# Optimization experiments

Measured on AMD Instinct MI355X. Metric: run time of the kernel, lower is better.

## Reference

```python
import jax, jax.numpy as jnp
import numpy as np

MAX_DISP = 4  # max_displacement = pad_size = 4, stride_1 = stride_2 = 1, kernel_size = 1
NEG_SLOPE = 0.1


def setup_inputs() -> dict:
    key = jax.random.key(0)
    k1, k2 = jax.random.split(key)
    B, C, H, W = 8, 128, 128, 256
    x1 = jax.random.normal(k1, (B, C, H, W), dtype=jnp.float32)
    x2 = jax.random.normal(k2, (B, C, H, W), dtype=jnp.float32)
    return {"x1": x1, "x2": x2}


def reference(x1, x2):
    # FlowNet/PWC-Net correlation: for each displacement (dy, dx) in
    # [-MAX_DISP, MAX_DISP]^2, dot-product over channels (normalized by C),
    # giving (2*MAX_DISP+1)^2 = 81 output channels; then LeakyReLU(0.1).
    B, C, H, W = x1.shape
    pad = MAX_DISP
    x2p = jnp.pad(x2, ((0, 0), (0, 0), (pad, pad), (pad, pad)))  # [B,C,H+8,W+8]
    vols = []
    for dy in range(2 * MAX_DISP + 1):          # fixed small displacement set
        for dx in range(2 * MAX_DISP + 1):
            shifted = jax.lax.dynamic_slice(x2p, (0, 0, dy, dx), (B, C, H, W))
            vols.append(jnp.mean(x1 * shifted, axis=1))  # mean over channels
    cv = jnp.stack(vols, axis=1)                 # [B, 81, H, W]
    return jax.nn.leaky_relu(cv, NEG_SLOPE)
```

## Files before the change

### kernel.cpp

```cpp
#include <hip/hip_runtime.h>


constexpr int MAXD = 4;
constexpr int ND   = 9;
constexpr int NDISP = 81;
constexpr int Bb = 8, Cc = 128, Hh = 128, Ww = 256;
constexpr int TH = 8, TW = 64, NPIX = 8;
constexpr int CK = 4;
constexpr int NCHUNK = Cc / CK;
constexpr int XROWS = TH + 2 * MAXD;
constexpr int XSTR  = 76;
constexpr int CH_TILE = XROWS * XSTR;
constexpr int BUFF = CK * CH_TILE;
constexpr int NTHREADS = ND * 64;
constexpr int HW = Hh * Ww;
constexpr float SCALE = 1.0f / 128.0f;
constexpr float SLOPE = 0.1f;

__global__ __launch_bounds__(NTHREADS, 1)
void corr81_kernel(const float* __restrict__ x1, const float* __restrict__ x2,
                   float* __restrict__ out) {
  const int tid = threadIdx.x;
  const int wv  = tid >> 6;
  const int l   = tid & 63;
  const int r   = l >> 3;
  const int cb  = (l & 7) << 3;

  const int w0 = blockIdx.x * TW;
  const int h0 = blockIdx.y * TH;
  const int b  = blockIdx.z;

  __shared__ float x2s[2 * BUFF];

  const int srow = tid / 36;
  const int scol = (tid - srow * 36) * 2;
  const int gh2  = h0 - MAXD + srow;
  const int gw2  = w0 - MAXD + scol;
  const bool sok = (gh2 >= 0) && (gh2 < Hh) && (gw2 >= 0) && (gw2 < Ww);
  const int x2base = b * (Cc * HW) + gh2 * Ww + gw2;
  const int sldso  = srow * XSTR + scol;

  const int x1base = (b * Cc * Hh + h0 + r) * Ww + w0 + cb;
  const int ldro   = (r + wv) * XSTR + cb;

  float acc[ND][NPIX];
#pragma unroll
  for (int dx = 0; dx < ND; ++dx)
#pragma unroll
    for (int i = 0; i < NPIX; ++i) acc[dx][i] = 0.0f;

  float a[2][NPIX];

  auto loadx1 = [&](int ch, float* dst) {
    const float* p = x1 + x1base + ch * HW;
    float4 t0 = *reinterpret_cast<const float4*>(p);
    float4 t1 = *reinterpret_cast<const float4*>(p + 4);
    dst[0] = t0.x; dst[1] = t0.y; dst[2] = t0.z; dst[3] = t0.w;
    dst[4] = t1.x; dst[5] = t1.y; dst[6] = t1.z; dst[7] = t1.w;
  };

#pragma unroll
  for (int c = 0; c < CK; ++c) {
    float2 v = make_float2(0.0f, 0.0f);
    if (sok) v = *reinterpret_cast<const float2*>(x2 + x2base + c * HW);
    *reinterpret_cast<float2*>(&x2s[c * CH_TILE + sldso]) = v;
  }
  loadx1(0, a[0]);
  __syncthreads();

  for (int k = 0; k < NCHUNK; ++k) {
    const int kn = k + 1;
    float2 sreg[CK];
    if (kn < NCHUNK) {
#pragma unroll
      for (int c = 0; c < CK; ++c) {
        float2 v = make_float2(0.0f, 0.0f);
        if (sok) v = *reinterpret_cast<const float2*>(x2 + x2base + (kn * CK + c) * HW);
        sreg[c] = v;
      }
    }
    const float* lb = &x2s[(k & 1) * BUFF + ldro];
#pragma unroll
    for (int c = 0; c < CK; ++c) {
      const int ch = k * CK + c;
      int chn = ch + 1; if (chn >= Cc) chn = Cc - 1;
      loadx1(chn, a[(c + 1) & 1]);

      const float* lp = lb + c * CH_TILE;
      float4 q0 = *reinterpret_cast<const float4*>(lp);
      float4 q1 = *reinterpret_cast<const float4*>(lp + 4);
      float4 q2 = *reinterpret_cast<const float4*>(lp + 8);
      float4 q3 = *reinterpret_cast<const float4*>(lp + 12);
      float xr[16] = {q0.x, q0.y, q0.z, q0.w, q1.x, q1.y, q1.z, q1.w,
                      q2.x, q2.y, q2.z, q2.w, q3.x, q3.y, q3.z, q3.w};
      const float* av = a[c & 1];
#pragma unroll
      for (int dx = 0; dx < ND; ++dx)
#pragma unroll
        for (int i = 0; i < NPIX; ++i)
          acc[dx][i] = fmaf(av[i], xr[i + dx], acc[dx][i]);
    }
    if (kn < NCHUNK) {
#pragma unroll
      for (int c = 0; c < CK; ++c)
        *reinterpret_cast<float2*>(&x2s[(kn & 1) * BUFF + c * CH_TILE + sldso]) = sreg[c];
    }
    __syncthreads();
  }

  const int obase = (b * NDISP + wv * ND) * HW + (h0 + r) * Ww + w0 + cb;
#pragma unroll
  for (int dx = 0; dx < ND; ++dx) {
    float4 v0, v1;
    float t;
    t = acc[dx][0] * SCALE; v0.x = fmaxf(t, t * SLOPE);
    t = acc[dx][1] * SCALE; v0.y = fmaxf(t, t * SLOPE);
    t = acc[dx][2] * SCALE; v0.z = fmaxf(t, t * SLOPE);
    t = acc[dx][3] * SCALE; v0.w = fmaxf(t, t * SLOPE);
    t = acc[dx][4] * SCALE; v1.x = fmaxf(t, t * SLOPE);
    t = acc[dx][5] * SCALE; v1.y = fmaxf(t, t * SLOPE);
    t = acc[dx][6] * SCALE; v1.z = fmaxf(t, t * SLOPE);
    t = acc[dx][7] * SCALE; v1.w = fmaxf(t, t * SLOPE);
    float* po = out + obase + dx * HW;
    *reinterpret_cast<float4*>(po)     = v0;
    *reinterpret_cast<float4*>(po + 4) = v1;
  }
}

extern "C" void kernel_launch(void* const* d_in, const int* in_sizes, int n_in,
                              void* d_out, int out_size, void* d_ws, size_t ws_size,
                              hipStream_t stream) {
  const float* x1 = (const float*)d_in[0];
  const float* x2 = (const float*)d_in[1];
  float* out = (float*)d_out;
  dim3 grid(Ww / TW, Hh / TH, Bb);
  corr81_kernel<<<grid, NTHREADS, 0, stream>>>(x1, x2, out);
}
```

Baseline: 419.6 us.

## Remap lanes, widen x2 staging to float4, batch x1 loads per chunk

Lane mapping is transposed so each wavefront's 8 row-lanes are contiguous, which changes the LDS access pattern across banks. x2 staging switches from float2 to float4 loads, with two thread groups each covering two channels, so fewer global and LDS transactions are issued. x1 loads for all four channels of a chunk are issued up front, LDS reads are double-buffered in registers, and sched_barriers pin the ordering. This raises register pressure and changes the bounds check at the right tile edge.

```diff
diff --git a/kernel.cpp b/kernel.cpp
--- a/kernel.cpp
+++ b/kernel.cpp
@@ -23,22 +23,25 @@
   const int tid = threadIdx.x;
   const int wv  = tid >> 6;
   const int l   = tid & 63;
-  const int r   = l >> 3;
-  const int cb  = (l & 7) << 3;
+  const int r   = l & 7;
+  const int cb  = (l >> 3) << 3;
 
   const int w0 = blockIdx.x * TW;
   const int h0 = blockIdx.y * TH;
   const int b  = blockIdx.z;
 
-  __shared__ float x2s[2 * BUFF];
+  __shared__ __align__(16) float x2s[2 * BUFF];
 
-  const int srow = tid / 36;
-  const int scol = (tid - srow * 36) * 2;
+  const int cp   = tid / 288;
+  const int st   = tid - cp * 288;
+  const int srow = st / 18;
+  const int scol = (st - srow * 18) * 4;
   const int gh2  = h0 - MAXD + srow;
   const int gw2  = w0 - MAXD + scol;
-  const bool sok = (gh2 >= 0) && (gh2 < Hh) && (gw2 >= 0) && (gw2 < Ww);
+  const bool sok = (gh2 >= 0) && (gh2 < Hh) && (gw2 >= 0) && (gw2 + 3 < Ww + 1);
   const int x2base = b * (Cc * HW) + gh2 * Ww + gw2;
   const int sldso  = srow * XSTR + scol;
+  const int chp0   = cp * 2;
 
   const int x1base = (b * Cc * Hh + h0 + r) * Ww + w0 + cb;
   const int ldro   = (r + wv) * XSTR + cb;
@@ -49,61 +52,70 @@
 #pragma unroll
     for (int i = 0; i < NPIX; ++i) acc[dx][i] = 0.0f;
 
-  float a[2][NPIX];
-
-  auto loadx1 = [&](int ch, float* dst) {
-    const float* p = x1 + x1base + ch * HW;
-    float4 t0 = *reinterpret_cast<const float4*>(p);
-    float4 t1 = *reinterpret_cast<const float4*>(p + 4);
-    dst[0] = t0.x; dst[1] = t0.y; dst[2] = t0.z; dst[3] = t0.w;
-    dst[4] = t1.x; dst[5] = t1.y; dst[6] = t1.z; dst[7] = t1.w;
+  auto ldx2 = [](const float* lp, float* dst) {
+    float4 q0 = *reinterpret_cast<const float4*>(lp);
+    float4 q1 = *reinterpret_cast<const float4*>(lp + 4);
+    float4 q2 = *reinterpret_cast<const float4*>(lp + 8);
+    float4 q3 = *reinterpret_cast<const float4*>(lp + 12);
+    dst[0]  = q0.x; dst[1]  = q0.y; dst[2]  = q0.z; dst[3]  = q0.w;
+    dst[4]  = q1.x; dst[5]  = q1.y; dst[6]  = q1.z; dst[7]  = q1.w;
+    dst[8]  = q2.x; dst[9]  = q2.y; dst[10] = q2.z; dst[11] = q2.w;
+    dst[12] = q3.x; dst[13] = q3.y; dst[14] = q3.z; dst[15] = q3.w;
   };
 
 #pragma unroll
-  for (int c = 0; c < CK; ++c) {
-    float2 v = make_float2(0.0f, 0.0f);
-    if (sok) v = *reinterpret_cast<const float2*>(x2 + x2base + c * HW);
-    *reinterpret_cast<float2*>(&x2s[c * CH_TILE + sldso]) = v;
+  for (int j = 0; j < 2; ++j) {
+    float4 v = make_float4(0.0f, 0.0f, 0.0f, 0.0f);
+    if (sok) v = *reinterpret_cast<const float4*>(x2 + x2base + (chp0 + j) * HW);
+    *reinterpret_cast<float4*>(&x2s[(chp0 + j) * CH_TILE + sldso]) = v;
   }
-  loadx1(0, a[0]);
   __syncthreads();
 
+#pragma unroll 1
   for (int k = 0; k < NCHUNK; ++k) {
     const int kn = k + 1;
-    float2 sreg[CK];
+
+    float a4[CK][NPIX];
+#pragma unroll
+    for (int c = 0; c < CK; ++c) {
+      const float* p = x1 + x1base + (k * CK + c) * HW;
+      float4 t0 = *reinterpret_cast<const float4*>(p);
+      float4 t1 = *reinterpret_cast<const float4*>(p + 4);
+      a4[c][0] = t0.x; a4[c][1] = t0.y; a4[c][2] = t0.z; a4[c][3] = t0.w;
+      a4[c][4] = t1.x; a4[c][5] = t1.y; a4[c][6] = t1.z; a4[c][7] = t1.w;
+    }
+    __builtin_amdgcn_sched_barrier(0);
+
+    float4 sreg[2];
     if (kn < NCHUNK) {
 #pragma unroll
-      for (int c = 0; c < CK; ++c) {
-        float2 v = make_float2(0.0f, 0.0f);
-        if (sok) v = *reinterpret_cast<const float2*>(x2 + x2base + (kn * CK + c) * HW);
-        sreg[c] = v;
+      for (int j = 0; j < 2; ++j) {
+        float4 v = make_float4(0.0f, 0.0f, 0.0f, 0.0f);
+        if (sok) v = *reinterpret_cast<const float4*>(x2 + x2base + (kn * CK + chp0 + j) * HW);
+        sreg[j] = v;
       }
     }
+    __builtin_amdgcn_sched_barrier(0);
+
     const float* lb = &x2s[(k & 1) * BUFF + ldro];
+    float xr[2][16];
+    ldx2(lb, xr[0]);
 #pragma unroll
     for (int c = 0; c < CK; ++c) {
-      const int ch = k * CK + c;
-      int chn = ch + 1; if (chn >= Cc) chn = Cc - 1;
-      loadx1(chn, a[(c + 1) & 1]);
-
-      const float* lp = lb + c * CH_TILE;
-      float4 q0 = *reinterpret_cast<const float4*>(lp);
-      float4 q1 = *reinterpret_cast<const float4*>(lp + 4);
-      float4 q2 = *reinterpret_cast<const float4*>(lp + 8);
-      float4 q3 = *reinterpret_cast<const float4*>(lp + 12);
-      float xr[16] = {q0.x, q0.y, q0.z, q0.w, q1.x, q1.y, q1.z, q1.w,
-                      q2.x, q2.y, q2.z, q2.w, q3.x, q3.y, q3.z, q3.w};
-      const float* av = a[c & 1];
+      if (c + 1 < CK) ldx2(lb + (c + 1) * CH_TILE, xr[(c + 1) & 1]);
+      const float* av = a4[c];
+      const float* xv = xr[c & 1];
 #pragma unroll
       for (int dx = 0; dx < ND; ++dx)
 #pragma unroll
         for (int i = 0; i < NPIX; ++i)
-          acc[dx][i] = fmaf(av[i], xr[i + dx], acc[dx][i]);
+          acc[dx][i] = fmaf(av[i], xv[i + dx], acc[dx][i]);
     }
+
     if (kn < NCHUNK) {
 #pragma unroll
-      for (int c = 0; c < CK; ++c)
-        *reinterpret_cast<float2*>(&x2s[(kn & 1) * BUFF + c * CH_TILE + sldso]) = sreg[c];
+      for (int j = 0; j < 2; ++j)
+        *reinterpret_cast<float4*>(&x2s[(kn & 1) * BUFF + (chp0 + j) * CH_TILE + sldso]) = sreg[j];
     }
     __syncthreads();
   }
```

After: 597.9 us. 42.5% more time.

## Load x2 windows directly from global memory, dropping LDS staging and barriers

Applied to the files above, without the earlier changes.

Removes the shared-memory double-buffered x2 tile and the per-chunk __syncthreads, and has each thread read its 16-wide x2 window straight from global memory with float4 loads, relying on L1/L2 for reuse across the 9 waves. Channels are software-pipelined two at a time in registers. This drops LDS traffic and block-wide synchronization, but it puts redundant global/cache loads on every wave, and float4 loads at offset cb-4 may be unaligned or zero-masked at the edges.

```diff
diff --git a/kernel.cpp b/kernel.cpp
--- a/kernel.cpp
+++ b/kernel.cpp
@@ -6,12 +6,6 @@
 constexpr int NDISP = 81;
 constexpr int Bb = 8, Cc = 128, Hh = 128, Ww = 256;
 constexpr int TH = 8, TW = 64, NPIX = 8;
-constexpr int CK = 4;
-constexpr int NCHUNK = Cc / CK;
-constexpr int XROWS = TH + 2 * MAXD;
-constexpr int XSTR  = 76;
-constexpr int CH_TILE = XROWS * XSTR;
-constexpr int BUFF = CK * CH_TILE;
 constexpr int NTHREADS = ND * 64;
 constexpr int HW = Hh * Ww;
 constexpr float SCALE = 1.0f / 128.0f;
@@ -30,18 +24,19 @@
   const int h0 = blockIdx.y * TH;
   const int b  = blockIdx.z;
 
-  __shared__ float x2s[2 * BUFF];
+  const int x1base = (b * Cc * Hh + h0 + r) * Ww + w0 + cb;
 
-  const int srow = tid / 36;
-  const int scol = (tid - srow * 36) * 2;
-  const int gh2  = h0 - MAXD + srow;
-  const int gw2  = w0 - MAXD + scol;
-  const bool sok = (gh2 >= 0) && (gh2 < Hh) && (gw2 >= 0) && (gw2 < Ww);
-  const int x2base = b * (Cc * HW) + gh2 * Ww + gw2;
-  const int sldso  = srow * XSTR + scol;
-
-  const int x1base = (b * Cc * Hh + h0 + r) * Ww + w0 + cb;
-  const int ldro   = (r + wv) * XSTR + cb;
+  const int gh2 = h0 + r + wv - MAXD;
+  const bool rowok = (gh2 >= 0) && (gh2 < Hh);
+  const int gw2 = w0 + cb - MAXD;
+  bool ok[4];
+#pragma unroll
+  for (int s = 0; s < 4; ++s) {
+    const int c0 = gw2 + 4 * s;
+    ok[s] = rowok && (c0 >= 0) && (c0 + 3 < Ww);
+  }
+  const int ghc = rowok ? gh2 : 0;
+  const int x2base = b * (Cc * HW) + ghc * Ww + gw2;
 
   float acc[ND][NPIX];
 #pragma unroll
@@ -49,64 +44,48 @@
 #pragma unroll
     for (int i = 0; i < NPIX; ++i) acc[dx][i] = 0.0f;
 
-  float a[2][NPIX];
-
-  auto loadx1 = [&](int ch, float* dst) {
+  auto ldx1 = [&](int ch, float* dst) {
     const float* p = x1 + x1base + ch * HW;
     float4 t0 = *reinterpret_cast<const float4*>(p);
     float4 t1 = *reinterpret_cast<const float4*>(p + 4);
     dst[0] = t0.x; dst[1] = t0.y; dst[2] = t0.z; dst[3] = t0.w;
     dst[4] = t1.x; dst[5] = t1.y; dst[6] = t1.z; dst[7] = t1.w;
   };
+  auto ldx2 = [&](int ch, float* dst) {
+    const float* p = x2 + x2base + ch * HW;
+#pragma unroll
+    for (int s = 0; s < 4; ++s) {
+      float4 q = make_float4(0.0f, 0.0f, 0.0f, 0.0f);
+      if (ok[s]) q = *reinterpret_cast<const float4*>(p + 4 * s);
+      dst[4 * s + 0] = q.x; dst[4 * s + 1] = q.y;
+      dst[4 * s + 2] = q.z; dst[4 * s + 3] = q.w;
+    }
+  };
 
-#pragma unroll
-  for (int c = 0; c < CK; ++c) {
-    float2 v = make_float2(0.0f, 0.0f);
-    if (sok) v = *reinterpret_cast<const float2*>(x2 + x2base + c * HW);
-    *reinterpret_cast<float2*>(&x2s[c * CH_TILE + sldso]) = v;
+  float a0[NPIX], a1[NPIX], xa[16], xb[16];
+
+#define FMA_BLOCK(av, xv)                                   \
+  _Pragma("unroll")                                         \
+  for (int dx = 0; dx < ND; ++dx)                           \
+    _Pragma("unroll")                                       \
+    for (int i = 0; i < NPIX; ++i)                          \
+      acc[dx][i] = fmaf((av)[i], (xv)[i + dx], acc[dx][i]);
+
+  ldx1(0, a0);
+  ldx2(0, xa);
+
+#pragma unroll 1
+  for (int ch = 0; ch < Cc; ch += 2) {
+    ldx1(ch + 1, a1);
+    ldx2(ch + 1, xb);
+    FMA_BLOCK(a0, xa)
+    if (ch + 2 < Cc) {
+      ldx1(ch + 2, a0);
+      ldx2(ch + 2, xa);
+    }
+    FMA_BLOCK(a1, xb)
   }
-  loadx1(0, a[0]);
-  __syncthreads();
-
-  for (int k = 0; k < NCHUNK; ++k) {
-    const int kn = k + 1;
-    float2 sreg[CK];
-    if (kn < NCHUNK) {
-#pragma unroll
-      for (int c = 0; c < CK; ++c) {
-        float2 v = make_float2(0.0f, 0.0f);
-        if (sok) v = *reinterpret_cast<const float2*>(x2 + x2base + (kn * CK + c) * HW);
-        sreg[c] = v;
-      }
-    }
-    const float* lb = &x2s[(k & 1) * BUFF + ldro];
-#pragma unroll
-    for (int c = 0; c < CK; ++c) {
-      const int ch = k * CK + c;
-      int chn = ch + 1; if (chn >= Cc) chn = Cc - 1;
-      loadx1(chn, a[(c + 1) & 1]);
-
-      const float* lp = lb + c * CH_TILE;
-      float4 q0 = *reinterpret_cast<const float4*>(lp);
-      float4 q1 = *reinterpret_cast<const float4*>(lp + 4);
-      float4 q2 = *reinterpret_cast<const float4*>(lp + 8);
-      float4 q3 = *reinterpret_cast<const float4*>(lp + 12);
-      float xr[16] = {q0.x, q0.y, q0.z, q0.w, q1.x, q1.y, q1.z, q1.w,
-                      q2.x, q2.y, q2.z, q2.w, q3.x, q3.y, q3.z, q3.w};
-      const float* av = a[c & 1];
-#pragma unroll
-      for (int dx = 0; dx < ND; ++dx)
-#pragma unroll
-        for (int i = 0; i < NPIX; ++i)
-          acc[dx][i] = fmaf(av[i], xr[i + dx], acc[dx][i]);
-    }
-    if (kn < NCHUNK) {
-#pragma unroll
-      for (int c = 0; c < CK; ++c)
-        *reinterpret_cast<float2*>(&x2s[(kn & 1) * BUFF + c * CH_TILE + sldso]) = sreg[c];
-    }
-    __syncthreads();
-  }
+#undef FMA_BLOCK
 
   const int obase = (b * NDISP + wv * ND) * HW + (h0 + r) * Ww + w0 + cb;
 #pragma unroll
```

Result: slower. 445.0 us (+6.0%).
